# Kernel tuning notes

Hardware: AMD Instinct MI355X
Metric: run time of the kernel (lower is better)

## Reference

```python
import jax, jax.numpy as jnp
import numpy as np

N_NODES = 50000
IN_CH = 256
N_REL = 5
N_EDGES = 800000
LAST_SENSES = 25000
LAST_GLOBALS = 45000


def setup_inputs() -> dict:
    key = jax.random.key(0)
    ks = jax.random.split(key, 12)
    batch_x = jax.random.normal(ks[0], (N_NODES, IN_CH), dtype=jnp.float32)
    batch_edge_index = jax.random.randint(ks[1], (2, N_EDGES), 0, N_NODES)
    batch_edge_type = jax.random.randint(ks[2], (N_EDGES,), 0, N_REL)
    s = 1.0 / np.sqrt(IN_CH)
    comp = jax.random.normal(ks[3], (N_REL, N_REL), dtype=jnp.float32) * (1.0 / np.sqrt(N_REL))
    basis = jax.random.normal(ks[4], (N_REL, IN_CH, IN_CH), dtype=jnp.float32) * s
    root = jax.random.normal(ks[5], (IN_CH, IN_CH), dtype=jnp.float32) * s
    bias = jnp.zeros((IN_CH,), dtype=jnp.float32)
    n_glob = LAST_GLOBALS - LAST_SENSES
    Wg = jax.random.normal(ks[6], (n_glob, IN_CH), dtype=jnp.float32) * s
    bg = jnp.zeros((n_glob,), dtype=jnp.float32)
    Ws = jax.random.normal(ks[7], (LAST_SENSES, IN_CH), dtype=jnp.float32) * s
    bs = jnp.zeros((LAST_SENSES,), dtype=jnp.float32)
    return {
        'batch_x': batch_x,
        'batch_edge_index': batch_edge_index,
        'batch_edge_type': batch_edge_type,
        'comp': comp,
        'basis': basis,
        'root': root,
        'bias': bias,
        'Wg': Wg,
        'bg': bg,
        'Ws': Ws,
        'bs': bs,
    }


def _rgcn_conv(x, edge_index, edge_type, comp, basis, root, bias):
    # Basis decomposition: W_r = sum_b comp[r,b] * basis[b]  -> [R, d, d]
    R = comp.shape[0]
    N = x.shape[0]
    W = jnp.einsum('rb,bdf->rdf', comp, basis)
    # Transform all nodes by every relation weight once ([R,N,F]), then gather
    # per edge instead of doing an [E,d,d] weight gather.
    H = jnp.einsum('nd,rdf->rnf', x, W)
    src, dst = edge_index[0], edge_index[1]
    msgs = H[edge_type, src]                     # [E, F]
    seg = edge_type * N + dst                    # combined (relation, dst) id
    sums = jax.ops.segment_sum(msgs, seg, num_segments=R * N)
    cnt = jax.ops.segment_sum(jnp.ones((msgs.shape[0],), msgs.dtype), seg,
                              num_segments=R * N)
    mean = sums / jnp.maximum(cnt, 1.0)[:, None]  # per-relation mean aggregation
    agg = mean.reshape(R, N, -1).sum(axis=0)
    return agg + x @ root + bias


def reference(batch_x, batch_edge_index, batch_edge_type, comp, basis, root,
              bias, Wg, bg, Ws, bs):
    h = jax.nn.relu(_rgcn_conv(batch_x, batch_edge_index, batch_edge_type,
                               comp, basis, root, bias))
    x1 = h[0]                                    # current node embedding [F]
    logits_global = Wg @ x1 + bg
    logits_sense = Ws @ x1 + bs
    return (jax.nn.log_softmax(logits_global, axis=0),
            jax.nn.log_softmax(logits_sense, axis=0))
```

## Files before the change

### kernel.cpp

```cpp
#include <hip/hip_runtime.h>
#include <math.h>

#define N_NODES 50000
#define IN_CH 256
#define N_REL 5
#define N_EDGES 800000
#define N_GLOB 20000
#define N_SENSE 25000
#define N_OUT 45000
#define MAX_MATCH 256
#define NBLK_LOGITS (N_OUT / 4)
#define NBLK_GLOB (N_GLOB / 4)


__device__ __forceinline__ void record_edge(const int* ei, const int* et,
                                            int* ip, int e) {
    int t = et[e];
    int p = atomicAdd(&ip[0], 1);
    if (p < MAX_MATCH) {
        ip[8 + p] = ei[e];
        ip[8 + MAX_MATCH + p] = t;
    }
    atomicAdd(&ip[1 + t], 1);
}

__global__ void k_scan(const int* __restrict__ ei,
                       const int* __restrict__ et,
                       int* __restrict__ ip) {
    int e4 = blockIdx.x * 256 + threadIdx.x;
    if (e4 * 4 >= N_EDGES) return;
    int4 d = ((const int4*)(ei + N_EDGES))[e4];
    int e = e4 * 4;
    if (d.x == 0) record_edge(ei, et, ip, e);
    if (d.y == 0) record_edge(ei, et, ip, e + 1);
    if (d.z == 0) record_edge(ei, et, ip, e + 2);
    if (d.w == 0) record_edge(ei, et, ip, e + 3);
}

__global__ __launch_bounds__(1024) void k_x1(const float* __restrict__ x,
                                             const float* __restrict__ comp,
                                             const float* __restrict__ basis,
                                             const float* __restrict__ root,
                                             const float* __restrict__ bias,
                                             const int* __restrict__ ip,
                                             float* __restrict__ x1acc) {
    __shared__ float u[IN_CH];
    __shared__ float red[4][IN_CH];
    int tid = threadIdx.x;
    int f = tid & 255, c = tid >> 8;
    int b = blockIdx.x;
    const float* M;
    if (b < 5) {
        if (c == 0) {
            int m = ip[0]; if (m > MAX_MATCH) m = MAX_MATCH;
            float acc = 0.f;
            for (int j = 0; j < m; ++j) {
                int s = ip[8 + j];
                int t = ip[8 + MAX_MATCH + j];
                float scale = comp[t * N_REL + b] /
                              fmaxf((float)ip[1 + t], 1.0f);
                acc += scale * x[(size_t)s * IN_CH + f];
            }
            u[f] = acc;
        }
        M = basis + (size_t)b * IN_CH * IN_CH;
    } else {
        if (c == 0) u[f] = x[f];
        M = root;
    }
    __syncthreads();
    const float* Mr = M + c * 64 * IN_CH;
    float acc = 0.f;
#pragma unroll 8
    for (int d = 0; d < 64; ++d) acc += u[c * 64 + d] * Mr[d * IN_CH + f];
    red[c][f] = acc;
    __syncthreads();
    if (c == 0) {
        float a = red[0][f] + red[1][f] + red[2][f] + red[3][f];
        if (b == 5) a += bias[f];
        atomicAdd(&x1acc[f], a);
    }
}

__global__ void k_logits(const float* __restrict__ Wg,
                         const float* __restrict__ bg,
                         const float* __restrict__ Ws,
                         const float* __restrict__ bs,
                         const float* __restrict__ x1acc,
                         float* __restrict__ out,
                         float* __restrict__ pmax,
                         float* __restrict__ psum) {
    __shared__ float sx[IN_CH];
    __shared__ float sl[4];
    int tid = threadIdx.x;
    sx[tid] = fmaxf(x1acc[tid], 0.f);
    __syncthreads();
    int lane = tid & 63, w = tid >> 6;
    int row = blockIdx.x * 4 + w;
    const float4* wr;
    float b;
    if (row < N_GLOB) {
        wr = (const float4*)(Wg + (size_t)row * IN_CH);
        b = bg[row];
    } else {
        int r2 = row - N_GLOB;
        wr = (const float4*)(Ws + (size_t)r2 * IN_CH);
        b = bs[r2];
    }
    float4 wv = wr[lane];
    float4 xv = ((const float4*)sx)[lane];
    float s = wv.x * xv.x + wv.y * xv.y + wv.z * xv.z + wv.w * xv.w;
#pragma unroll
    for (int off = 32; off > 0; off >>= 1) s += __shfl_down(s, off);
    if (lane == 0) { float l = s + b; out[row] = l; sl[w] = l; }
    __syncthreads();
    if (tid == 0) {
        float m4 = fmaxf(fmaxf(sl[0], sl[1]), fmaxf(sl[2], sl[3]));
        float s4 = expf(sl[0] - m4) + expf(sl[1] - m4) +
                   expf(sl[2] - m4) + expf(sl[3] - m4);
        pmax[blockIdx.x] = m4;
        psum[blockIdx.x] = s4;
    }
}

__global__ void k_statsfinal(const float* __restrict__ pmax,
                             const float* __restrict__ psum,
                             float* __restrict__ out) {
    __shared__ float rmg[256], rsg[256], rms[256], rss[256];
    int tid = threadIdx.x;
    float mg = -3.4e38f, sg = 0.f, ms = -3.4e38f, ss = 0.f;
    for (int i = tid; i < NBLK_LOGITS; i += 256) {
        float mi = pmax[i], si = psum[i];
        if (i < NBLK_GLOB) {
            float M = fmaxf(mg, mi);
            sg = sg * expf(mg - M) + si * expf(mi - M); mg = M;
        } else {
            float M = fmaxf(ms, mi);
            ss = ss * expf(ms - M) + si * expf(mi - M); ms = M;
        }
    }
    rmg[tid] = mg; rsg[tid] = sg; rms[tid] = ms; rss[tid] = ss;
    __syncthreads();
    for (int h = 128; h > 0; h >>= 1) {
        if (tid < h) {
            float m2 = rmg[tid + h], s2 = rsg[tid + h];
            float M = fmaxf(rmg[tid], m2);
            rsg[tid] = rsg[tid] * expf(rmg[tid] - M) + s2 * expf(m2 - M);
            rmg[tid] = M;
            m2 = rms[tid + h]; s2 = rss[tid + h];
            M = fmaxf(rms[tid], m2);
            rss[tid] = rss[tid] * expf(rms[tid] - M) + s2 * expf(m2 - M);
            rms[tid] = M;
        }
        __syncthreads();
    }
    float zg = rmg[0] + logf(rsg[0]);
    float zs = rms[0] + logf(rss[0]);
    int row = blockIdx.x * 256 + tid;
    if (row < N_OUT) out[row] -= (row < N_GLOB) ? zg : zs;
}

extern "C" void kernel_launch(void* const* d_in, const int* in_sizes, int n_in,
                              void* d_out, int out_size, void* d_ws, size_t ws_size,
                              hipStream_t stream) {
    const float* x     = (const float*)d_in[0];
    const int*   ei    = (const int*)  d_in[1];
    const int*   et    = (const int*)  d_in[2];
    const float* comp  = (const float*)d_in[3];
    const float* basis = (const float*)d_in[4];
    const float* root  = (const float*)d_in[5];
    const float* bias  = (const float*)d_in[6];
    const float* Wg    = (const float*)d_in[7];
    const float* bg    = (const float*)d_in[8];
    const float* Wsn   = (const float*)d_in[9];
    const float* bs    = (const float*)d_in[10];
    float* out = (float*)d_out;

    float* base  = (float*)d_ws;
    float* x1acc = base;
    int*   ip    = (int*)(base + 256);
    float* pmax  = base + 1024;
    float* psum  = base + 12274;

    hipMemsetAsync(d_ws, 0, 264 * sizeof(float), stream);
    k_scan      <<<(N_EDGES / 4 + 255) / 256, 256, 0, stream>>>(ei, et, ip);
    k_x1        <<<6, 1024, 0, stream>>>(x, comp, basis, root, bias, ip, x1acc);
    k_logits    <<<NBLK_LOGITS, 256, 0, stream>>>(Wg, bg, Wsn, bs, x1acc, out, pmax, psum);
    k_statsfinal<<<(N_OUT + 255) / 256, 256, 0, stream>>>(pmax, psum, out);
}
```

Before: 169.1 us.

## Split x1 matvec across more blocks, grid-stride logits, two-pass softmax stats

k_x1 now runs as 24 blocks of 256 threads, each handling a 64-row slice of one matrix, instead of 6 blocks of 1024 threads with a shared-memory reduction. k_logits becomes a grid-stride loop over 2048 blocks that writes raw logits, with no per-block max/sum partials. k_statsfinal recomputes max and sum-exp over all raw logits in every block in two passes, then writes normalized float4 outputs. This spreads the x1 work over more CUs and cuts launch size, but each final block now rereads the whole 180KB logits array redundantly.

New measurement: 170.8 us. No clear change (+1.0%).

```diff
diff --git a/kernel.cpp b/kernel.cpp
--- a/kernel.cpp
+++ b/kernel.cpp
@@ -9,8 +9,10 @@
 #define N_SENSE 25000
 #define N_OUT 45000
 #define MAX_MATCH 256
-#define NBLK_LOGITS (N_OUT / 4)
-#define NBLK_GLOB (N_GLOB / 4)
+#define LOGIT_BLOCKS 2048
+#define NWAVES (LOGIT_BLOCKS * 4)
+#define N_OUT4 (N_OUT / 4)
+#define N_GLOB4 (N_GLOB / 4)
 
 
 __device__ __forceinline__ void record_edge(const int* ei, const int* et,
@@ -37,49 +39,41 @@
     if (d.w == 0) record_edge(ei, et, ip, e + 3);
 }
 
-__global__ __launch_bounds__(1024) void k_x1(const float* __restrict__ x,
-                                             const float* __restrict__ comp,
-                                             const float* __restrict__ basis,
-                                             const float* __restrict__ root,
-                                             const float* __restrict__ bias,
-                                             const int* __restrict__ ip,
-                                             float* __restrict__ x1acc) {
-    __shared__ float u[IN_CH];
-    __shared__ float red[4][IN_CH];
+__global__ void k_x1(const float* __restrict__ x,
+                     const float* __restrict__ comp,
+                     const float* __restrict__ basis,
+                     const float* __restrict__ root,
+                     const float* __restrict__ bias,
+                     const int* __restrict__ ip,
+                     float* __restrict__ x1acc) {
+    __shared__ float u[64];
     int tid = threadIdx.x;
-    int f = tid & 255, c = tid >> 8;
-    int b = blockIdx.x;
-    const float* M;
-    if (b < 5) {
-        if (c == 0) {
+    int mat = blockIdx.x >> 2;
+    int d0 = (blockIdx.x & 3) * 64;
+    if (tid < 64) {
+        if (mat < 5) {
             int m = ip[0]; if (m > MAX_MATCH) m = MAX_MATCH;
             float acc = 0.f;
             for (int j = 0; j < m; ++j) {
                 int s = ip[8 + j];
                 int t = ip[8 + MAX_MATCH + j];
-                float scale = comp[t * N_REL + b] /
+                float scale = comp[t * N_REL + mat] /
                               fmaxf((float)ip[1 + t], 1.0f);
-                acc += scale * x[(size_t)s * IN_CH + f];
+                acc += scale * x[(size_t)s * IN_CH + d0 + tid];
             }
-            u[f] = acc;
+            u[tid] = acc;
+        } else {
+            u[tid] = x[d0 + tid];
         }
-        M = basis + (size_t)b * IN_CH * IN_CH;
-    } else {
-        if (c == 0) u[f] = x[f];
-        M = root;
     }
     __syncthreads();
-    const float* Mr = M + c * 64 * IN_CH;
+    const float* M = ((mat < 5) ? (basis + (size_t)mat * IN_CH * IN_CH)
+                                : root) + (size_t)d0 * IN_CH;
     float acc = 0.f;
-#pragma unroll 8
-    for (int d = 0; d < 64; ++d) acc += u[c * 64 + d] * Mr[d * IN_CH + f];
-    red[c][f] = acc;
-    __syncthreads();
-    if (c == 0) {
-        float a = red[0][f] + red[1][f] + red[2][f] + red[3][f];
-        if (b == 5) a += bias[f];
-        atomicAdd(&x1acc[f], a);
-    }
+#pragma unroll 16
+    for (int d = 0; d < 64; ++d) acc += u[d] * M[d * IN_CH + tid];
+    if (mat == 5 && d0 == 0) acc += bias[tid];
+    atomicAdd(&x1acc[tid], acc);
 }
 
 __global__ void k_logits(const float* __restrict__ Wg,
@@ -87,77 +81,73 @@
                          const float* __restrict__ Ws,
                          const float* __restrict__ bs,
                          const float* __restrict__ x1acc,
-                         float* __restrict__ out,
-                         float* __restrict__ pmax,
-                         float* __restrict__ psum) {
-    __shared__ float sx[IN_CH];
-    __shared__ float sl[4];
-    int tid = threadIdx.x;
-    sx[tid] = fmaxf(x1acc[tid], 0.f);
-    __syncthreads();
-    int lane = tid & 63, w = tid >> 6;
-    int row = blockIdx.x * 4 + w;
-    const float4* wr;
-    float b;
-    if (row < N_GLOB) {
-        wr = (const float4*)(Wg + (size_t)row * IN_CH);
-        b = bg[row];
-    } else {
-        int r2 = row - N_GLOB;
-        wr = (const float4*)(Ws + (size_t)r2 * IN_CH);
-        b = bs[r2];
-    }
-    float4 wv = wr[lane];
-    float4 xv = ((const float4*)sx)[lane];
-    float s = wv.x * xv.x + wv.y * xv.y + wv.z * xv.z + wv.w * xv.w;
+                         float* __restrict__ raw) {
+    int tid = threadIdx.x, lane = tid & 63;
+    int gw = blockIdx.x * 4 + (tid >> 6);
+    float4 xv = ((const float4*)x1acc)[lane];
+    xv.x = fmaxf(xv.x, 0.f); xv.y = fmaxf(xv.y, 0.f);
+    xv.z = fmaxf(xv.z, 0.f); xv.w = fmaxf(xv.w, 0.f);
+    for (int row = gw; row < N_OUT; row += NWAVES) {
+        const float4* wr;
+        float b;
+        if (row < N_GLOB) {
+            wr = (const float4*)(Wg + (size_t)row * IN_CH);
+            b = bg[row];
+        } else {
+            int r2 = row - N_GLOB;
+            wr = (const float4*)(Ws + (size_t)r2 * IN_CH);
+            b = bs[r2];
+        }
+        float4 wv = wr[lane];
+        float s = wv.x * xv.x + wv.y * xv.y + wv.z * xv.z + wv.w * xv.w;
 #pragma unroll
-    for (int off = 32; off > 0; off >>= 1) s += __shfl_down(s, off);
-    if (lane == 0) { float l = s + b; out[row] = l; sl[w] = l; }
-    __syncthreads();
-    if (tid == 0) {
-        float m4 = fmaxf(fmaxf(sl[0], sl[1]), fmaxf(sl[2], sl[3]));
-        float s4 = expf(sl[0] - m4) + expf(sl[1] - m4) +
-                   expf(sl[2] - m4) + expf(sl[3] - m4);
-        pmax[blockIdx.x] = m4;
-        psum[blockIdx.x] = s4;
+        for (int off = 32; off > 0; off >>= 1) s += __shfl_down(s, off);
+        if (lane == 0) raw[row] = s + b;
     }
 }
 
-__global__ void k_statsfinal(const float* __restrict__ pmax,
-                             const float* __restrict__ psum,
+__global__ void k_statsfinal(const float* __restrict__ raw,
                              float* __restrict__ out) {
-    __shared__ float rmg[256], rsg[256], rms[256], rss[256];
+    __shared__ float r1[256], r2[256];
     int tid = threadIdx.x;
-    float mg = -3.4e38f, sg = 0.f, ms = -3.4e38f, ss = 0.f;
-    for (int i = tid; i < NBLK_LOGITS; i += 256) {
-        float mi = pmax[i], si = psum[i];
-        if (i < NBLK_GLOB) {
-            float M = fmaxf(mg, mi);
-            sg = sg * expf(mg - M) + si * expf(mi - M); mg = M;
-        } else {
-            float M = fmaxf(ms, mi);
-            ss = ss * expf(ms - M) + si * expf(mi - M); ms = M;
-        }
+    const float4* o4 = (const float4*)raw;
+    float mg = -3.4e38f, ms = -3.4e38f;
+    for (int i = tid; i < N_OUT4; i += 256) {
+        float4 v = o4[i];
+        float m4 = fmaxf(fmaxf(v.x, v.y), fmaxf(v.z, v.w));
+        if (i < N_GLOB4) mg = fmaxf(mg, m4); else ms = fmaxf(ms, m4);
     }
-    rmg[tid] = mg; rsg[tid] = sg; rms[tid] = ms; rss[tid] = ss;
-    __syncthreads();
+    r1[tid] = mg; r2[tid] = ms; __syncthreads();
     for (int h = 128; h > 0; h >>= 1) {
         if (tid < h) {
-            float m2 = rmg[tid + h], s2 = rsg[tid + h];
-            float M = fmaxf(rmg[tid], m2);
-            rsg[tid] = rsg[tid] * expf(rmg[tid] - M) + s2 * expf(m2 - M);
-            rmg[tid] = M;
-            m2 = rms[tid + h]; s2 = rss[tid + h];
-            M = fmaxf(rms[tid], m2);
-            rss[tid] = rss[tid] * expf(rms[tid] - M) + s2 * expf(m2 - M);
-            rms[tid] = M;
+            r1[tid] = fmaxf(r1[tid], r1[tid + h]);
+            r2[tid] = fmaxf(r2[tid], r2[tid + h]);
         }
         __syncthreads();
     }
-    float zg = rmg[0] + logf(rsg[0]);
-    float zs = rms[0] + logf(rss[0]);
-    int row = blockIdx.x * 256 + tid;
-    if (row < N_OUT) out[row] -= (row < N_GLOB) ? zg : zs;
+    mg = r1[0]; ms = r2[0]; __syncthreads();
+    float sg = 0.f, ss = 0.f;
+    for (int i = tid; i < N_OUT4; i += 256) {
+        float4 v = o4[i];
+        if (i < N_GLOB4)
+            sg += expf(v.x - mg) + expf(v.y - mg) + expf(v.z - mg) + expf(v.w - mg);
+        else
+            ss += expf(v.x - ms) + expf(v.y - ms) + expf(v.z - ms) + expf(v.w - ms);
+    }
+    r1[tid] = sg; r2[tid] = ss; __syncthreads();
+    for (int h = 128; h > 0; h >>= 1) {
+        if (tid < h) { r1[tid] += r1[tid + h]; r2[tid] += r2[tid + h]; }
+        __syncthreads();
+    }
+    float zg = mg + logf(r1[0]);
+    float zs = ms + logf(r2[0]);
+    int i = blockIdx.x * 256 + tid;
+    if (i < N_OUT4) {
+        float4 v = o4[i];
+        float z = (i < N_GLOB4) ? zg : zs;
+        v.x -= z; v.y -= z; v.z -= z; v.w -= z;
+        ((float4*)out)[i] = v;
+    }
 }
 
 extern "C" void kernel_launch(void* const* d_in, const int* in_sizes, int n_in,
@@ -179,12 +169,11 @@
     float* base  = (float*)d_ws;
     float* x1acc = base;
     int*   ip    = (int*)(base + 256);
-    float* pmax  = base + 1024;
-    float* psum  = base + 12274;
+    float* raw   = base + 1024;
 
-    hipMemsetAsync(d_ws, 0, 264 * sizeof(float), stream);
+    hipMemsetAsync(d_ws, 0, 1056, stream);
     k_scan      <<<(N_EDGES / 4 + 255) / 256, 256, 0, stream>>>(ei, et, ip);
-    k_x1        <<<6, 1024, 0, stream>>>(x, comp, basis, root, bias, ip, x1acc);
-    k_logits    <<<NBLK_LOGITS, 256, 0, stream>>>(Wg, bg, Wsn, bs, x1acc, out, pmax, psum);
-    k_statsfinal<<<(N_OUT + 255) / 256, 256, 0, stream>>>(pmax, psum, out);
+    k_x1        <<<24, 256, 0, stream>>>(x, comp, basis, root, bias, ip, x1acc);
+    k_logits    <<<LOGIT_BLOCKS, 256, 0, stream>>>(Wg, bg, Wsn, bs, x1acc, raw);
+    k_statsfinal<<<(N_OUT4 + 255) / 256, 256, 0, stream>>>(raw, out);
 }
```
